# Performance work log

Hardware: AMD Instinct MI355X
Metric: run time of the kernel (lower is better)

Reference implementation:

```python
import jax, jax.numpy as jnp
import numpy as np

BN_EPS = 1e-5


def setup_inputs() -> dict:
    key = jax.random.key(0)
    ks = jax.random.split(key, 5)
    b, c, h, w = 4, 256, 64, 64
    pre = jax.random.normal(ks[0], (b, c, h, w), dtype=jnp.float32)
    cur = jax.random.normal(ks[1], (b, c, h, w), dtype=jnp.float32)
    # 1x1 conv weight stored as [out_ch, in_ch] (kernel is 1x1)
    W = jax.random.normal(ks[2], (256, 2 * c), dtype=jnp.float32) * (1.0 / np.sqrt(2 * c))
    b_conv = jax.random.normal(ks[3], (256,), dtype=jnp.float32) * 0.01
    gamma = jnp.ones((256,), dtype=jnp.float32)
    beta = jnp.zeros((256,), dtype=jnp.float32)
    run_mean = jnp.zeros((256,), dtype=jnp.float32)
    run_var = jnp.ones((256,), dtype=jnp.float32)
    alpha = jnp.full((1,), 0.25, dtype=jnp.float32)  # PReLU single shared slope
    return {"pre": pre, "cur": cur, "W": W, "b_conv": b_conv, "gamma": gamma,
            "beta": beta, "run_mean": run_mean, "run_var": run_var, "alpha": alpha}


def reference(pre, cur, W, b_conv, gamma, beta, run_mean, run_var, alpha):
    b, c, h, w = cur.shape
    hw = h * w
    pre_a = pre.reshape(b, c, hw)            # [b, c, hw]
    cur_a = cur.reshape(b, c, hw)            # [b, c, hw]
    # scores[b, i, j] = sum_c pre[b,c,i] * cur[b,c,j]
    scores = jnp.einsum('bci,bcj->bij', pre_a, cur_a)
    attn = jax.nn.softmax(scores * (c ** -0.5), axis=-1)   # [b, hw, hw]
    # feat[b, c, i] = sum_j attn[b,i,j] * cur[b,c,j]
    feat = jnp.einsum('bij,bcj->bci', attn, cur_a)          # [b, c, hw]
    x = jnp.concatenate([feat, cur_a], axis=1).reshape(b, 2 * c, h, w)
    # 1x1 conv
    y = jnp.einsum('bchw,oc->bohw', x, W) + b_conv[None, :, None, None]
    # BatchNorm2d (inference: running stats)
    inv = gamma * jax.lax.rsqrt(run_var + BN_EPS)
    y = y * inv[None, :, None, None] + (beta - run_mean * inv)[None, :, None, None]
    # PReLU (single shared parameter)
    a = alpha[0]
    return jnp.where(y >= 0, y, a * y)
```

## Files before the change

### kernel.cpp

```cpp
#include <hip/hip_runtime.h>
#include <hip/hip_bf16.h>
#include <math.h>

#define HWX 4096
#define CCH 256
#define NB  4

typedef __attribute__((ext_vector_type(8))) short short8;
typedef __attribute__((ext_vector_type(4))) short short4v;
typedef __attribute__((ext_vector_type(4))) float f32x4;
typedef __attribute__((ext_vector_type(2))) float f32x2;

#define WS_QT 0ull
#define WS_KT 8388608ull
#define WS_V  16777216ull
#define WS_W  25165824ull
#define WS_FT 25427968ull
#define WS_PO 33816576ull

__device__ __forceinline__ short f2bf(float f) {
  union { float f; unsigned u; } a; a.f = f;
  unsigned r = a.u + 0x7FFFu + ((a.u >> 16) & 1u);
  return (short)(r >> 16);
}

__device__ __forceinline__ float bf2f(short s) {
  union { unsigned u; float f; } a;
  a.u = ((unsigned)(unsigned short)s) << 16;
  return a.f;
}

__device__ __forceinline__ short f2bf_rn(float f) {
  __hip_bfloat16 h = __float2bfloat16(f);
  return *reinterpret_cast<short*>(&h);
}

__device__ __forceinline__ f32x4 mfma16(short8 a, short8 b, f32x4 c) {
  return __builtin_amdgcn_mfma_f32_16x16x32_bf16(a, b, c, 0, 0, 0);
}

__device__ __forceinline__ void gload16(const void* g, void* l) {
  __builtin_amdgcn_global_load_lds(
      (const __attribute__((address_space(1))) unsigned int*)g,
      (__attribute__((address_space(3))) unsigned int*)l, 16, 0, 0);
}

__global__ __launch_bounds__(256) void prep_qkv(const float* __restrict__ pre,
                                                const float* __restrict__ cur,
                                                char* __restrict__ ws) {
  __shared__ short ldsT[256 * 36];
  const int tid = threadIdx.x;
  const int b  = blockIdx.x >> 7;
  const int jt = blockIdx.x & 127;
  const int j0 = jt * 32;
  const float* preB = pre + (size_t)b * CCH * HWX + j0;
  const float* curB = cur + (size_t)b * CCH * HWX + j0;
  char* vout = ws + WS_V  + (size_t)(b * 128 + jt) * 16384;
  char* kout = ws + WS_KT + (size_t)(b * 128 + jt) * 16384;
  char* qout = ws + WS_QT + (size_t)(b * 128 + jt) * 16384;

  short v[32];
  {
    const float* p = curB + (size_t)tid * HWX;
#pragma unroll
    for (int k = 0; k < 8; ++k) {
      f32x4 f = *(const f32x4*)(p + k * 4);
      v[k*4+0] = f2bf(f[0]); v[k*4+1] = f2bf(f[1]);
      v[k*4+2] = f2bf(f[2]); v[k*4+3] = f2bf(f[3]);
    }
  }
#pragma unroll
  for (int k = 0; k < 4; ++k) {
    short8 o8;
#pragma unroll
    for (int e = 0; e < 8; ++e) o8[e] = v[k * 8 + e];
    *(short8*)(vout + ((tid * 64 + k * 16) ^ ((tid & 7) << 4))) = o8;
  }
#pragma unroll
  for (int j = 0; j < 32; ++j) ldsT[tid * 36 + j] = v[j];
  __syncthreads();
  {
    const int j = tid >> 3, m = tid & 7;
#pragma unroll
    for (int k = 0; k < 4; ++k) {
      short8 o8;
#pragma unroll
      for (int e = 0; e < 8; ++e) o8[e] = ldsT[(m * 32 + k * 8 + e) * 36 + j];
      *(short8*)(kout + ((j * 512 + m * 64 + k * 16) ^ ((j & 7) << 4))) = o8;
    }
  }
  __syncthreads();
  {
    const float* p = preB + (size_t)tid * HWX;
#pragma unroll
    for (int k = 0; k < 8; ++k) {
      f32x4 f = *(const f32x4*)(p + k * 4);
      v[k*4+0] = f2bf(f[0]); v[k*4+1] = f2bf(f[1]);
      v[k*4+2] = f2bf(f[2]); v[k*4+3] = f2bf(f[3]);
    }
  }
#pragma unroll
  for (int j = 0; j < 32; ++j) ldsT[tid * 36 + j] = v[j];
  __syncthreads();
  {
    const int j = tid >> 3, m = tid & 7;
#pragma unroll
    for (int k = 0; k < 4; ++k) {
      short8 o8;
#pragma unroll
      for (int e = 0; e < 8; ++e) o8[e] = ldsT[(m * 32 + k * 8 + e) * 36 + j];
      *(short8*)(qout + ((j * 512 + m * 64 + k * 16) ^ ((j & 7) << 4))) = o8;
    }
  }
}

__global__ __launch_bounds__(256) void prep_w(const float* __restrict__ Wm,
                                              char* __restrict__ ws) {
  const int sl = blockIdx.x;
  const int o  = threadIdx.x;
  char* out = ws + WS_W + (size_t)sl * 32768;
  const float* src = Wm + (size_t)o * 512 + sl * 64;
  short tmp[64];
#pragma unroll
  for (int k = 0; k < 16; ++k) {
    f32x4 f = *(const f32x4*)(src + k * 4);
    tmp[k*4+0] = f2bf(f[0]); tmp[k*4+1] = f2bf(f[1]);
    tmp[k*4+2] = f2bf(f[2]); tmp[k*4+3] = f2bf(f[3]);
  }
#pragma unroll
  for (int k = 0; k < 8; ++k) {
    short8 o8;
#pragma unroll
    for (int e = 0; e < 8; ++e) o8[e] = tmp[k * 8 + e];
    *(short8*)(out + ((o * 128 + k * 16) ^ ((o & 7) << 4))) = o8;
  }
}

template <int S>
__global__ __launch_bounds__(128, 2) void attn_sb(char* __restrict__ ws) {
  __shared__ __align__(16) char smem[37888];
  const int tid = threadIdx.x, lane = tid & 63, wv = tid >> 6;
  const int g = lane >> 4, l15 = lane & 15;
  const int p = blockIdx.x;
  const int NT = 128 / S;
  int b, s, it;
  if (S == 4) {
    const int L = (p & 7) * 128 + (p >> 3);
    b = L >> 8; s = (L >> 6) & 3; it = L & 63;
  } else if (S == 2) {
    const int L = (p & 7) * 64 + (p >> 3);
    b = L >> 7; s = (L >> 6) & 1; it = L & 63;
  } else {
    const int L = (p & 7) * 32 + (p >> 3);
    b = L >> 6; s = 0; it = L & 63;
  }
  const int i0 = it * 64;
  const char* qimg  = ws + WS_QT + (size_t)(b * 128 + it * 2) * 16384;
  const char* kbase = ws + WS_KT + (size_t)(b * 128 + s * NT) * 16384;
  const char* vbase = ws + WS_V  + (size_t)(b * 128 + s * NT) * 16384;

#pragma unroll
  for (int k = 0; k < 16; ++k)
    gload16(qimg + k * 2048 + tid * 16, smem + k * 2048 + tid * 16);
  __syncthreads();
  short8 qf[2][8];
  {
    const char* qt = smem + wv * 16384;
#pragma unroll
    for (int qsub = 0; qsub < 2; ++qsub)
#pragma unroll
      for (int kb = 0; kb < 8; ++kb)
        qf[qsub][kb] = *(const short8*)(qt + (qsub * 16 + l15) * 512 +
                                        ((kb * 64 + g * 16) ^ ((l15 & 7) << 4)));
  }
  __syncthreads();

  f32x4 acc[2][16];
#pragma unroll
  for (int qsub = 0; qsub < 2; ++qsub)
#pragma unroll
    for (int nt = 0; nt < 16; ++nt) acc[qsub][nt] = (f32x4){0.f, 0.f, 0.f, 0.f};
  f32x4 accl[2];
  accl[0] = (f32x4){0.f, 0.f, 0.f, 0.f};
  accl[1] = (f32x4){0.f, 0.f, 0.f, 0.f};
  const float SL2E = 1.4426950408889634f / 16.0f;
  short8 ones;
#pragma unroll
  for (int e = 0; e < 8; ++e) ones[e] = (short)16256;

#pragma unroll
  for (int k = 0; k < 8; ++k) {
    gload16(kbase + k * 2048 + tid * 16, smem + k * 2048 + tid * 16);
    gload16(vbase + k * 2048 + tid * 16, smem + 16384 + k * 2048 + tid * 16);
  }
  __syncthreads();

  short* pw = (short*)(smem + 32768 + wv * 2560);
  for (int t = 0; t < NT; ++t) {
    const char* bk = smem;
    const char* bv = smem + 16384;
    f32x4 s00 = (f32x4){0.f,0.f,0.f,0.f}, s01 = (f32x4){0.f,0.f,0.f,0.f};
    f32x4 s10 = (f32x4){0.f,0.f,0.f,0.f}, s11 = (f32x4){0.f,0.f,0.f,0.f};
    __builtin_amdgcn_s_setprio(1);
#pragma unroll
    for (int kb = 0; kb < 8; ++kb) {
      const int co = (kb * 64 + g * 16) ^ ((l15 & 7) << 4);
      short8 k0 = *(const short8*)(bk + l15 * 512 + co);
      short8 k1 = *(const short8*)(bk + (l15 + 16) * 512 + co);
      s00 = mfma16(qf[0][kb], k0, s00);
      s01 = mfma16(qf[0][kb], k1, s01);
      s10 = mfma16(qf[1][kb], k0, s10);
      s11 = mfma16(qf[1][kb], k1, s11);
    }
    __builtin_amdgcn_s_setprio(0);
#pragma unroll
    for (int r = 0; r < 4; ++r) {
      pw[(g * 4 + r) * 40 + l15]           = f2bf_rn(exp2f(fmaf(s00[r], SL2E, -16.0f)));
      pw[(g * 4 + r) * 40 + 16 + l15]      = f2bf_rn(exp2f(fmaf(s01[r], SL2E, -16.0f)));
      pw[(16 + g * 4 + r) * 40 + l15]      = f2bf_rn(exp2f(fmaf(s10[r], SL2E, -16.0f)));
      pw[(16 + g * 4 + r) * 40 + 16 + l15] = f2bf_rn(exp2f(fmaf(s11[r], SL2E, -16.0f)));
    }
    short8 pf0 = *(const short8*)((const char*)pw + l15 * 80 + g * 16);
    short8 pf1 = *(const short8*)((const char*)pw + (16 + l15) * 80 + g * 16);
    __builtin_amdgcn_s_setprio(1);
    accl[0] = mfma16(pf0, ones, accl[0]);
    accl[1] = mfma16(pf1, ones, accl[1]);
#pragma unroll
    for (int nt = 0; nt < 16; ++nt) {
      const int c = nt * 16 + l15;
      short8 vf = *(const short8*)(bv + ((c * 64 + g * 16) ^ ((c & 7) << 4)));
      acc[0][nt] = mfma16(pf0, vf, acc[0][nt]);
      acc[1][nt] = mfma16(pf1, vf, acc[1][nt]);
    }
    __builtin_amdgcn_s_setprio(0);
    __syncthreads();
    if (t + 1 < NT) {
      const char* ks = kbase + (size_t)(t + 1) * 16384;
      const char* vs = vbase + (size_t)(t + 1) * 16384;
#pragma unroll
      for (int k = 0; k < 8; ++k) {
        gload16(ks + k * 2048 + tid * 16, smem + k * 2048 + tid * 16);
        gload16(vs + k * 2048 + tid * 16, smem + 16384 + k * 2048 + tid * 16);
      }
    }
    __syncthreads();
  }

  short* po = (short*)(ws + WS_PO) + (size_t)(s * NB + b) * CCH * HWX;
#pragma unroll
  for (int qsub = 0; qsub < 2; ++qsub)
#pragma unroll
    for (int nt = 0; nt < 16; ++nt) {
      const int c = nt * 16 + l15;
      short4v o4;
#pragma unroll
      for (int r = 0; r < 4; ++r) o4[r] = f2bf_rn(acc[qsub][nt][r]);
      *(short4v*)(po + (size_t)c * HWX + i0 + wv * 32 + qsub * 16 + g * 4) = o4;
    }
  if (l15 == 0) {
    short* pl = (short*)(ws + WS_PO + (size_t)S * 8388608ull) +
                (size_t)(s * NB + b) * HWX + i0 + wv * 32 + g * 4;
    short4v a4, b4;
#pragma unroll
    for (int r = 0; r < 4; ++r) { a4[r] = f2bf_rn(accl[0][r]); b4[r] = f2bf_rn(accl[1][r]); }
    *(short4v*)pl = a4;
    *(short4v*)(pl + 16) = b4;
  }
}

template <int S>
__global__ __launch_bounds__(256) void merge_feat(char* __restrict__ ws) {
  __shared__ float linv[32];
  __shared__ short ldsT[32 * 66];
  const int tid = threadIdx.x;
  const int p = blockIdx.x;
  const int L = (p & 7) * 64 + (p >> 3);
  const int b = L >> 7, it = L & 127, i0 = it * 32;
  const short* po = (const short*)(ws + WS_PO);
  const short* pl = (const short*)(ws + WS_PO + (size_t)S * 8388608ull);
  if (tid < 32) {
    float l = 0.0f;
#pragma unroll
    for (int s = 0; s < S; ++s)
      l += bf2f(pl[(size_t)(s * NB + b) * HWX + i0 + tid]);
    linv[tid] = 1.0f / l;
  }
  __syncthreads();
  char* fout = ws + WS_FT + (size_t)(b * 128 + it) * 16384;
#pragma unroll
  for (int ch = 0; ch < 4; ++ch) {
    const int c = ch * 64 + (tid >> 2);
    const int qo = (tid & 3) * 8;
    float a[8];
#pragma unroll
    for (int e = 0; e < 8; ++e) a[e] = 0.0f;
#pragma unroll
    for (int s = 0; s < S; ++s) {
      short8 v8 = *(const short8*)(po + (size_t)(s * NB + b) * CCH * HWX +
                                   (size_t)c * HWX + i0 + qo);
#pragma unroll
      for (int e = 0; e < 8; ++e) a[e] += bf2f(v8[e]);
    }
#pragma unroll
    for (int e = 0; e < 8; ++e)
      ldsT[(qo + e) * 66 + (tid >> 2)] = f2bf(a[e] * linv[qo + e]);
    __syncthreads();
    {
      const int i = tid >> 3, m = tid & 7;
      short8 o8;
#pragma unroll
      for (int e = 0; e < 8; ++e) o8[e] = ldsT[i * 66 + m * 8 + e];
      *(short8*)(fout + ((i * 512 + ch * 128 + m * 16) ^ ((i & 7) << 4))) = o8;
    }
    __syncthreads();
  }
}

__global__ __launch_bounds__(256) void conv_mfma(const float* __restrict__ bconv,
                                                 const float* __restrict__ gamma,
                                                 const float* __restrict__ beta,
                                                 const float* __restrict__ rmean,
                                                 const float* __restrict__ rvar,
                                                 const float* __restrict__ alpha,
                                                 char* __restrict__ ws,
                                                 float* __restrict__ out) {
  __shared__ __align__(16) char smem[73728];
  const int tid = threadIdx.x, lane = tid & 63, wv = tid >> 6;
  const int g = lane >> 4, l15 = lane & 15;
  const int p = blockIdx.x;
  const int L = (p & 7) * 64 + (p >> 3);
  const int b = L >> 7, it = L & 127, i0 = it * 32;
  const char* wimg = ws + WS_W;
  const char* ft = ws + WS_FT + (size_t)(b * 128 + it) * 16384;
  const char* kt = ws + WS_KT + (size_t)(b * 128 + it) * 16384;

  f32x4 acc[4][2];
#pragma unroll
  for (int ot = 0; ot < 4; ++ot)
#pragma unroll
    for (int itt = 0; itt < 2; ++itt) acc[ot][itt] = (f32x4){0.f, 0.f, 0.f, 0.f};

  const int xi = wv * 8 + (lane >> 3), xw = (lane & 7) * 16;

#pragma unroll
  for (int k = 0; k < 8; ++k)
    gload16(wimg + wv * 8192 + k * 1024 + lane * 16,
            smem + wv * 8192 + k * 1024 + lane * 16);
  gload16(ft + xi * 512 + xw, smem + 65536 + wv * 1024 + lane * 16);
  __syncthreads();

  int cur = 0;
  for (int st = 0; st < 8; ++st) {
    if (st < 7) {
      const int sn = st + 1;
      const char* img = (sn < 4) ? ft : kt;
      const int coff = (sn & 3) * 128;
#pragma unroll
      for (int k = 0; k < 8; ++k)
        gload16(wimg + (size_t)sn * 32768 + wv * 8192 + k * 1024 + lane * 16,
                smem + (cur ^ 1) * 32768 + wv * 8192 + k * 1024 + lane * 16);
      gload16(img + xi * 512 + coff + xw,
              smem + 65536 + (cur ^ 1) * 4096 + wv * 1024 + lane * 16);
    }
    const char* wb = smem + cur * 32768;
    const char* xb = smem + 65536 + cur * 4096;
    short8 bx[2][2];
#pragma unroll
    for (int itt = 0; itt < 2; ++itt) {
      const int i = itt * 16 + l15;
#pragma unroll
      for (int kb = 0; kb < 2; ++kb)
        bx[itt][kb] = *(const short8*)(xb + i * 128 + ((kb * 64 + g * 16) ^ ((i & 7) << 4)));
    }
#pragma unroll
    for (int ot = 0; ot < 4; ++ot) {
      const int o = wv * 64 + ot * 16 + l15;
#pragma unroll
      for (int kb = 0; kb < 2; ++kb) {
        short8 aw = *(const short8*)(wb + o * 128 + ((kb * 64 + g * 16) ^ ((o & 7) << 4)));
#pragma unroll
        for (int itt = 0; itt < 2; ++itt)
          acc[ot][itt] = mfma16(aw, bx[itt][kb], acc[ot][itt]);
      }
    }
    __syncthreads();
    cur ^= 1;
  }

  const float a0 = alpha[0];
  float* outB = out + (size_t)b * CCH * HWX;
#pragma unroll
  for (int ot = 0; ot < 4; ++ot)
#pragma unroll
    for (int r = 0; r < 4; ++r) {
      const int o = wv * 64 + ot * 16 + g * 4 + r;
      const float inv = gamma[o] * rsqrtf(rvar[o] + 1e-5f);
      const float add = beta[o] - rmean[o] * inv + bconv[o] * inv;
#pragma unroll
      for (int itt = 0; itt < 2; ++itt) {
        float v = acc[ot][itt][r] * inv + add;
        v = (v >= 0.0f) ? v : a0 * v;
        outB[(size_t)o * HWX + i0 + itt * 16 + l15] = v;
      }
    }
}

__global__ __launch_bounds__(256) void legacy_attn(const float* __restrict__ pre,
                                                   const float* __restrict__ cur,
                                                   float* __restrict__ feat) {
  __shared__ __align__(16) char smem[43008];
  short* lds_q  = (short*)smem;
  short* lds_kT = (short*)smem;
  short* lds_v  = (short*)(smem + 16896);
  short* lds_p  = (short*)(smem + 37376);
  const int tid = threadIdx.x, lane = tid & 63, wv = tid >> 6;
  const int b = blockIdx.x >> 6, i0 = (blockIdx.x & 63) * 64;
  const float* preB = pre + (size_t)b * CCH * HWX;
  const float* curB = cur + (size_t)b * CCH * HWX;
  float* featB = feat + (size_t)b * CCH * HWX;
  {
    const int ib = (tid & 15) * 4, cbb = (tid >> 4) * 4;
#pragma unroll
    for (int p = 0; p < 4; ++p) {
      const int c = cbb + 64 * p;
      f32x4 f[4];
#pragma unroll
      for (int r = 0; r < 4; ++r)
        f[r] = *(const f32x4*)(preB + (size_t)(c + r) * HWX + i0 + ib);
#pragma unroll
      for (int e = 0; e < 4; ++e) {
        short4v s2;
        s2[0] = f2bf(f[0][e]); s2[1] = f2bf(f[1][e]);
        s2[2] = f2bf(f[2][e]); s2[3] = f2bf(f[3][e]);
        *(short4v*)(&lds_q[(ib + e) * 264 + c]) = s2;
      }
    }
  }
  __syncthreads();
  short8 qf[8];
  {
    const int r = wv * 16 + (lane & 15), ko = (lane >> 4) * 8;
#pragma unroll
    for (int kb = 0; kb < 8; ++kb)
      qf[kb] = *(const short8*)(&lds_q[r * 264 + kb * 32 + ko]);
  }
  f32x4 acc[16];
#pragma unroll
  for (int nt = 0; nt < 16; ++nt) acc[nt] = (f32x4){0.f, 0.f, 0.f, 0.f};
  float m_run[4], l_run[4];
#pragma unroll
  for (int r = 0; r < 4; ++r) { m_run[r] = -1e30f; l_run[r] = 0.0f; }
  const float SL2E = 1.4426950408889634f / 16.0f;
  for (int jt = 0; jt < 128; ++jt) {
    const int j0 = jt * 32;
    __syncthreads();
    {
      const int jb = (tid & 7) * 4, cbb = (tid >> 3) * 4;
#pragma unroll
      for (int p = 0; p < 2; ++p) {
        const int c = cbb + 128 * p;
        f32x4 f[4];
#pragma unroll
        for (int r = 0; r < 4; ++r)
          f[r] = *(const f32x4*)(curB + (size_t)(c + r) * HWX + j0 + jb);
#pragma unroll
        for (int r = 0; r < 4; ++r) {
          short4v s2;
          s2[0] = f2bf(f[r][0]); s2[1] = f2bf(f[r][1]);
          s2[2] = f2bf(f[r][2]); s2[3] = f2bf(f[r][3]);
          *(short4v*)(&lds_v[(c + r) * 40 + jb]) = s2;
        }
#pragma unroll
        for (int e = 0; e < 4; ++e) {
          short4v s2;
          s2[0] = f2bf(f[0][e]); s2[1] = f2bf(f[1][e]);
          s2[2] = f2bf(f[2][e]); s2[3] = f2bf(f[3][e]);
          *(short4v*)(&lds_kT[(jb + e) * 264 + c]) = s2;
        }
      }
    }
    __syncthreads();
    f32x4 s0 = (f32x4){0.f,0.f,0.f,0.f}, s1 = (f32x4){0.f,0.f,0.f,0.f};
    {
      const int jc = lane & 15, ko = (lane >> 4) * 8;
#pragma unroll
      for (int kb = 0; kb < 8; ++kb) {
        short8 k0 = *(const short8*)(&lds_kT[jc * 264 + kb * 32 + ko]);
        short8 k1 = *(const short8*)(&lds_kT[(jc + 16) * 264 + kb * 32 + ko]);
        s0 = mfma16(qf[kb], k0, s0);
        s1 = mfma16(qf[kb], k1, s1);
      }
    }
    float p0[4], p1[4], corr[4];
#pragma unroll
    for (int r = 0; r < 4; ++r) {
      float t = fmaxf(s0[r], s1[r]);
      t = fmaxf(t, __shfl_xor(t, 1)); t = fmaxf(t, __shfl_xor(t, 2));
      t = fmaxf(t, __shfl_xor(t, 4)); t = fmaxf(t, __shfl_xor(t, 8));
      const float mn = fmaxf(m_run[r], t * SL2E);
      corr[r] = exp2f(m_run[r] - mn);
      m_run[r] = mn;
      p0[r] = exp2f(s0[r] * SL2E - mn);
      p1[r] = exp2f(s1[r] * SL2E - mn);
      float rs = p0[r] + p1[r];
      rs += __shfl_xor(rs, 1); rs += __shfl_xor(rs, 2);
      rs += __shfl_xor(rs, 4); rs += __shfl_xor(rs, 8);
      l_run[r] = l_run[r] * corr[r] + rs;
    }
#pragma unroll
    for (int nt = 0; nt < 16; ++nt)
#pragma unroll
      for (int r = 0; r < 4; ++r) acc[nt][r] *= corr[r];
    {
      short* pw = lds_p + wv * 640;
      const int g = lane >> 4, jc = lane & 15;
#pragma unroll
      for (int r = 0; r < 4; ++r) {
        pw[(g * 4 + r) * 40 + jc]      = f2bf(p0[r]);
        pw[(g * 4 + r) * 40 + 16 + jc] = f2bf(p1[r]);
      }
    }
    {
      const int g = lane >> 4, rr = lane & 15;
      short8 pf = *(const short8*)(&lds_p[wv * 640 + rr * 40 + g * 8]);
#pragma unroll
      for (int nt = 0; nt < 16; ++nt) {
        short8 vf = *(const short8*)(&lds_v[(nt * 16 + rr) * 40 + g * 8]);
        acc[nt] = mfma16(pf, vf, acc[nt]);
      }
    }
  }
  {
    const int g = lane >> 4, jc = lane & 15;
    float rl[4];
#pragma unroll
    for (int r = 0; r < 4; ++r) rl[r] = 1.0f / l_run[r];
#pragma unroll
    for (int nt = 0; nt < 16; ++nt) {
      const int c = nt * 16 + jc;
#pragma unroll
      for (int r = 0; r < 4; ++r)
        featB[(size_t)c * HWX + i0 + wv * 16 + g * 4 + r] = acc[nt][r] * rl[r];
    }
  }
}

__global__ __launch_bounds__(256) void legacy_conv(const float* feat,
                                                   const float* __restrict__ cur,
                                                   const float* __restrict__ Wm,
                                                   const float* __restrict__ bconv,
                                                   const float* __restrict__ gamma,
                                                   const float* __restrict__ beta,
                                                   const float* __restrict__ rmean,
                                                   const float* __restrict__ rvar,
                                                   const float* __restrict__ alpha,
                                                   float* out) {
  __shared__ __align__(16) char smem[25600];
  short* lds_w = (short*)smem;
  short* lds_x = (short*)(smem + 20480);
  const int tid = threadIdx.x, lane = tid & 63, wv = tid >> 6;
  const int b = blockIdx.x >> 6, i0 = (blockIdx.x & 63) * 64;
  const float* featB = feat + (size_t)b * CCH * HWX;
  const float* curB  = cur  + (size_t)b * CCH * HWX;
  f32x4 acc[4][4];
#pragma unroll
  for (int ot = 0; ot < 4; ++ot)
#pragma unroll
    for (int it = 0; it < 4; ++it) acc[ot][it] = (f32x4){0.f, 0.f, 0.f, 0.f};
  for (int ks = 0; ks < 16; ++ks) {
    const int k0 = ks * 32;
    __syncthreads();
    {
      const int kq = (tid & 7) * 4, ob = tid >> 3;
#pragma unroll
      for (int p = 0; p < 8; ++p) {
        const int o = ob + 32 * p;
        f32x4 f = *(const f32x4*)(Wm + (size_t)o * 512 + k0 + kq);
        short4v s2;
        s2[0] = f2bf(f[0]); s2[1] = f2bf(f[1]); s2[2] = f2bf(f[2]); s2[3] = f2bf(f[3]);
        *(short4v*)(&lds_w[o * 40 + kq]) = s2;
      }
    }
    {
      const int i2 = (tid & 31) * 2, cc = ((tid >> 5) & 7) * 4;
      const float* basep = (k0 < 256) ? (featB + (size_t)(k0 + cc) * HWX)
                                      : (curB + (size_t)(k0 + cc - 256) * HWX);
      f32x2 f[4];
#pragma unroll
      for (int r = 0; r < 4; ++r)
        f[r] = *(const f32x2*)(basep + (size_t)r * HWX + i0 + i2);
#pragma unroll
      for (int e = 0; e < 2; ++e) {
        short4v s2;
        s2[0] = f2bf(f[0][e]); s2[1] = f2bf(f[1][e]);
        s2[2] = f2bf(f[2][e]); s2[3] = f2bf(f[3][e]);
        *(short4v*)(&lds_x[(i2 + e) * 40 + cc]) = s2;
      }
    }
    __syncthreads();
    {
      const int g = lane >> 4, rr = lane & 15;
      short8 af[4], bx[4];
#pragma unroll
      for (int ot = 0; ot < 4; ++ot)
        af[ot] = *(const short8*)(&lds_w[(wv * 64 + ot * 16 + rr) * 40 + g * 8]);
#pragma unroll
      for (int it = 0; it < 4; ++it)
        bx[it] = *(const short8*)(&lds_x[(it * 16 + rr) * 40 + g * 8]);
#pragma unroll
      for (int ot = 0; ot < 4; ++ot)
#pragma unroll
        for (int it = 0; it < 4; ++it)
          acc[ot][it] = mfma16(af[ot], bx[it], acc[ot][it]);
    }
  }
  const float a0 = alpha[0];
  const int g = lane >> 4, ic = lane & 15;
  float* outB = out + (size_t)b * CCH * HWX;
#pragma unroll
  for (int ot = 0; ot < 4; ++ot)
#pragma unroll
    for (int r = 0; r < 4; ++r) {
      const int o = wv * 64 + ot * 16 + g * 4 + r;
      const float inv = gamma[o] * rsqrtf(rvar[o] + 1e-5f);
      const float add = beta[o] - rmean[o] * inv + bconv[o] * inv;
#pragma unroll
      for (int it = 0; it < 4; ++it) {
        float v = acc[ot][it][r] * inv + add;
        v = (v >= 0.0f) ? v : a0 * v;
        outB[(size_t)o * HWX + i0 + it * 16 + ic] = v;
      }
    }
}

extern "C" void kernel_launch(void* const* d_in, const int* in_sizes, int n_in,
                              void* d_out, int out_size, void* d_ws, size_t ws_size,
                              hipStream_t stream) {
  (void)in_sizes; (void)n_in; (void)out_size;
  const float* pre   = (const float*)d_in[0];
  const float* cur   = (const float*)d_in[1];
  const float* Wm    = (const float*)d_in[2];
  const float* bconv = (const float*)d_in[3];
  const float* gamma = (const float*)d_in[4];
  const float* beta  = (const float*)d_in[5];
  const float* rmean = (const float*)d_in[6];
  const float* rvar  = (const float*)d_in[7];
  const float* alpha = (const float*)d_in[8];
  float* out = (float*)d_out;
  char* ws = (char*)d_ws;

  const size_t need4 = WS_PO + 4ull * (8388608ull + 32768ull);
  const size_t need2 = WS_PO + 2ull * (8388608ull + 32768ull);
  const size_t need1 = WS_PO + 1ull * (8388608ull + 32768ull);

  if (ws_size >= need1) {
    prep_qkv<<<dim3(512), dim3(256), 0, stream>>>(pre, cur, ws);
    prep_w<<<dim3(8), dim3(256), 0, stream>>>(Wm, ws);
    if (ws_size >= need4) {
      attn_sb<4><<<dim3(1024), dim3(128), 0, stream>>>(ws);
      merge_feat<4><<<dim3(512), dim3(256), 0, stream>>>(ws);
    } else if (ws_size >= need2) {
      attn_sb<2><<<dim3(512), dim3(128), 0, stream>>>(ws);
      merge_feat<2><<<dim3(512), dim3(256), 0, stream>>>(ws);
    } else {
      attn_sb<1><<<dim3(256), dim3(128), 0, stream>>>(ws);
      merge_feat<1><<<dim3(512), dim3(256), 0, stream>>>(ws);
    }
    conv_mfma<<<dim3(512), dim3(256), 0, stream>>>(bconv, gamma, beta, rmean,
                                                   rvar, alpha, ws, out);
  } else {
    legacy_attn<<<dim3(256), dim3(256), 0, stream>>>(pre, cur, out);
    legacy_conv<<<dim3(256), dim3(256), 0, stream>>>(out, cur, Wm, bconv, gamma,
                                                     beta, rmean, rvar, alpha, out);
  }
}
```

Before: 141.3 us.

## Add double-buffered 4-wave attention kernel with larger query tile for split-4 path

Adds a new attention kernel, attn_db4, for the 4-way key split. It uses 256 threads (4 waves) covering 128 query rows per block instead of 2 waves over 64, so each K/V tile loaded into shared memory is reused by twice as many query rows. K/V tiles are double-buffered: the next tile is loaded while the current one is computed, with one barrier per iteration. The grid halves to 512 blocks, and shared memory use grows to about 74 KB per block, which may limit occupancy.

Measured after the change: 137.7 us. 2.6% less time.

```diff
diff --git a/kernel.cpp b/kernel.cpp
--- a/kernel.cpp
+++ b/kernel.cpp
@@ -136,6 +136,130 @@
   }
 }
 
+__global__ __launch_bounds__(256, 2) void attn_db4(char* __restrict__ ws) {
+  __shared__ __align__(16) char smem[75776];
+  const int tid = threadIdx.x, lane = tid & 63, wv = tid >> 6;
+  const int g = lane >> 4, l15 = lane & 15;
+  const int p = blockIdx.x;
+  const int L = (p & 7) * 64 + (p >> 3);
+  const int b = L >> 7, s = (L >> 5) & 3, it = L & 31;
+  const int i0 = it * 128;
+  const int NT = 32;
+  const char* qimg  = ws + WS_QT + (size_t)(b * 128 + it * 4) * 16384;
+  const char* kbase = ws + WS_KT + (size_t)(b * 128 + s * NT) * 16384;
+  const char* vbase = ws + WS_V  + (size_t)(b * 128 + s * NT) * 16384;
+
+#pragma unroll
+  for (int k = 0; k < 16; ++k)
+    gload16(qimg + k * 4096 + tid * 16, smem + k * 4096 + tid * 16);
+  __syncthreads();
+  short8 qf[2][8];
+  {
+    const char* qt = smem + wv * 16384;
+#pragma unroll
+    for (int qsub = 0; qsub < 2; ++qsub)
+#pragma unroll
+      for (int kb = 0; kb < 8; ++kb)
+        qf[qsub][kb] = *(const short8*)(qt + (qsub * 16 + l15) * 512 +
+                                        ((kb * 64 + g * 16) ^ ((l15 & 7) << 4)));
+  }
+  __syncthreads();
+
+  f32x4 acc[2][16];
+#pragma unroll
+  for (int qsub = 0; qsub < 2; ++qsub)
+#pragma unroll
+    for (int nt = 0; nt < 16; ++nt) acc[qsub][nt] = (f32x4){0.f, 0.f, 0.f, 0.f};
+  f32x4 accl[2];
+  accl[0] = (f32x4){0.f, 0.f, 0.f, 0.f};
+  accl[1] = (f32x4){0.f, 0.f, 0.f, 0.f};
+  const float SL2E = 1.4426950408889634f / 16.0f;
+  short8 ones;
+#pragma unroll
+  for (int e = 0; e < 8; ++e) ones[e] = (short)16256;
+
+#pragma unroll
+  for (int k = 0; k < 4; ++k) {
+    gload16(kbase + k * 4096 + tid * 16, smem + k * 4096 + tid * 16);
+    gload16(vbase + k * 4096 + tid * 16, smem + 16384 + k * 4096 + tid * 16);
+  }
+  __syncthreads();
+
+  short* pw = (short*)(smem + 65536 + wv * 2560);
+  int cur = 0;
+  for (int t = 0; t < NT; ++t) {
+    if (t + 1 < NT) {
+      const char* ks = kbase + (size_t)(t + 1) * 16384;
+      const char* vs = vbase + (size_t)(t + 1) * 16384;
+      char* dst = smem + (cur ^ 1) * 32768 + tid * 16;
+#pragma unroll
+      for (int k = 0; k < 4; ++k) {
+        gload16(ks + k * 4096 + tid * 16, dst + k * 4096);
+        gload16(vs + k * 4096 + tid * 16, dst + 16384 + k * 4096);
+      }
+    }
+    const char* bk = smem + cur * 32768;
+    const char* bv = bk + 16384;
+    f32x4 s00 = (f32x4){0.f,0.f,0.f,0.f}, s01 = (f32x4){0.f,0.f,0.f,0.f};
+    f32x4 s10 = (f32x4){0.f,0.f,0.f,0.f}, s11 = (f32x4){0.f,0.f,0.f,0.f};
+    __builtin_amdgcn_s_setprio(1);
+#pragma unroll
+    for (int kb = 0; kb < 8; ++kb) {
+      const int co = (kb * 64 + g * 16) ^ ((l15 & 7) << 4);
+      short8 k0 = *(const short8*)(bk + l15 * 512 + co);
+      short8 k1 = *(const short8*)(bk + (l15 + 16) * 512 + co);
+      s00 = mfma16(qf[0][kb], k0, s00);
+      s01 = mfma16(qf[0][kb], k1, s01);
+      s10 = mfma16(qf[1][kb], k0, s10);
+      s11 = mfma16(qf[1][kb], k1, s11);
+    }
+    __builtin_amdgcn_s_setprio(0);
+#pragma unroll
+    for (int r = 0; r < 4; ++r) {
+      pw[(g * 4 + r) * 40 + l15]           = f2bf_rn(exp2f(fmaf(s00[r], SL2E, -16.0f)));
+      pw[(g * 4 + r) * 40 + 16 + l15]      = f2bf_rn(exp2f(fmaf(s01[r], SL2E, -16.0f)));
+      pw[(16 + g * 4 + r) * 40 + l15]      = f2bf_rn(exp2f(fmaf(s10[r], SL2E, -16.0f)));
+      pw[(16 + g * 4 + r) * 40 + 16 + l15] = f2bf_rn(exp2f(fmaf(s11[r], SL2E, -16.0f)));
+    }
+    short8 pf0 = *(const short8*)((const char*)pw + l15 * 80 + g * 16);
+    short8 pf1 = *(const short8*)((const char*)pw + (16 + l15) * 80 + g * 16);
+    __builtin_amdgcn_s_setprio(1);
+    accl[0] = mfma16(pf0, ones, accl[0]);
+    accl[1] = mfma16(pf1, ones, accl[1]);
+#pragma unroll
+    for (int nt = 0; nt < 16; ++nt) {
+      const int c = nt * 16 + l15;
+      short8 vf = *(const short8*)(bv + ((c * 64 + g * 16) ^ ((c & 7) << 4)));
+      acc[0][nt] = mfma16(pf0, vf, acc[0][nt]);
+      acc[1][nt] = mfma16(pf1, vf, acc[1][nt]);
+    }
+    __builtin_amdgcn_s_setprio(0);
+    __syncthreads();
+    cur ^= 1;
+  }
+
+  short* po = (short*)(ws + WS_PO) + (size_t)(s * NB + b) * CCH * HWX;
+#pragma unroll
+  for (int qsub = 0; qsub < 2; ++qsub)
+#pragma unroll
+    for (int nt = 0; nt < 16; ++nt) {
+      const int c = nt * 16 + l15;
+      short4v o4;
+#pragma unroll
+      for (int r = 0; r < 4; ++r) o4[r] = f2bf_rn(acc[qsub][nt][r]);
+      *(short4v*)(po + (size_t)c * HWX + i0 + wv * 32 + qsub * 16 + g * 4) = o4;
+    }
+  if (l15 == 0) {
+    short* pl = (short*)(ws + WS_PO + 4ull * 8388608ull) +
+                (size_t)(s * NB + b) * HWX + i0 + wv * 32 + g * 4;
+    short4v a4, b4;
+#pragma unroll
+    for (int r = 0; r < 4; ++r) { a4[r] = f2bf_rn(accl[0][r]); b4[r] = f2bf_rn(accl[1][r]); }
+    *(short4v*)pl = a4;
+    *(short4v*)(pl + 16) = b4;
+  }
+}
+
 template <int S>
 __global__ __launch_bounds__(128, 2) void attn_sb(char* __restrict__ ws) {
   __shared__ __align__(16) char smem[37888];
@@ -144,10 +268,7 @@
   const int p = blockIdx.x;
   const int NT = 128 / S;
   int b, s, it;
-  if (S == 4) {
-    const int L = (p & 7) * 128 + (p >> 3);
-    b = L >> 8; s = (L >> 6) & 3; it = L & 63;
-  } else if (S == 2) {
+  if (S == 2) {
     const int L = (p & 7) * 64 + (p >> 3);
     b = L >> 7; s = (L >> 6) & 1; it = L & 63;
   } else {
@@ -657,7 +778,7 @@
     prep_qkv<<<dim3(512), dim3(256), 0, stream>>>(pre, cur, ws);
     prep_w<<<dim3(8), dim3(256), 0, stream>>>(Wm, ws);
     if (ws_size >= need4) {
-      attn_sb<4><<<dim3(1024), dim3(128), 0, stream>>>(ws);
+      attn_db4<<<dim3(512), dim3(256), 0, stream>>>(ws);
       merge_feat<4><<<dim3(512), dim3(256), 0, stream>>>(ws);
     } else if (ws_size >= need2) {
       attn_sb<2><<<dim3(512), dim3(128), 0, stream>>>(ws);
```
